# Optimization experiments

Measured on AMD Instinct MI355X. Metric: run time of the kernel, lower is better.

Reference implementation:

```python
import jax, jax.numpy as jnp
import numpy as np
import math

CHUNK = 128


def setup_inputs() -> dict:
    key = jax.random.key(0)
    ks = jax.random.split(key, 12)
    B, S, H, D = 2, 4096, 1024, 2048  # D = hidden_dim * expansion_factor
    std = 0.02
    inp = {
        "hidden_states": jax.random.normal(ks[0], (B, S, H), jnp.float32),
        "Wq": jax.random.normal(ks[1], (H, D), jnp.float32) * std,
        "bq": jnp.zeros((D,), jnp.float32),
        "Wk": jax.random.normal(ks[2], (H, D), jnp.float32) * std,
        "bk": jnp.zeros((D,), jnp.float32),
        "Wv": jax.random.normal(ks[3], (H, D), jnp.float32) * std,
        "bv": jnp.zeros((D,), jnp.float32),
        "Wg": jax.random.normal(ks[4], (H, D), jnp.float32) * std,
        "bg": jnp.zeros((D,), jnp.float32),
        "Wo": jax.random.normal(ks[5], (D, H), jnp.float32) * std,
        "bo": jnp.zeros((H,), jnp.float32),
    }
    return inp


def reference(hidden_states, Wq, bq, Wk, bk, Wv, bv, Wg, bg, Wo, bo):
    B, S, H = hidden_states.shape
    D = Wq.shape[1]
    cs = CHUNK
    nC = S // cs  # seq_len chosen as multiple of chunk_size (no padding path)

    q = hidden_states @ Wq + bq
    k = hidden_states @ Wk + bk
    v = hidden_states @ Wv + bv
    gate = jax.nn.sigmoid(hidden_states @ Wg + bg)

    qc = q.reshape(B, nC, cs, D)
    kc = k.reshape(B, nC, cs, D)
    vc = v.reshape(B, nC, cs, D)
    gc = gate.reshape(B, nC, cs, D)

    # intra-chunk causal softmax attention (vectorized over all chunks)
    scale = 1.0 / math.sqrt(D)
    attn = jnp.einsum('bncd,bnkd->bnck', qc, kc) * scale  # [B,nC,cs,cs]
    causal = jnp.tril(jnp.ones((cs, cs), bool))
    attn = jnp.where(causal, attn, -jnp.inf)
    attn = jax.nn.softmax(attn, axis=-1)
    local = jnp.einsum('bnck,bnkd->bncd', attn, vc)

    # inter-chunk linear-attention state accumulation:
    # cross_i = q_i @ sum_{j<i} K_j^T V_j  (sequential scan over chunks)
    def step(state, xs):
        qi, ki, vi = xs  # each [B,cs,D]
        cross = jnp.einsum('bcd,bde->bce', qi, state)
        state = state + jnp.einsum('bcd,bce->bde', ki, vi)
        return state, cross

    state0 = jnp.zeros((B, D, D), hidden_states.dtype)
    _, cross = jax.lax.scan(
        step, state0,
        (qc.transpose(1, 0, 2, 3), kc.transpose(1, 0, 2, 3), vc.transpose(1, 0, 2, 3)))
    cross = cross.transpose(1, 0, 2, 3)  # [B,nC,cs,D]

    out = (local + cross) * gc
    out = out.reshape(B, S, D)
    return out @ Wo + bo
```

## Files before the change

kernel.cpp:

```cpp
#include <hip/hip_runtime.h>
#include <hip/hip_bf16.h>
#include <math.h>


typedef __bf16 bf16_t;
typedef __bf16 bf16x8 __attribute__((ext_vector_type(8)));
typedef __bf16 bf16x4 __attribute__((ext_vector_type(4)));
typedef float f32x4 __attribute__((ext_vector_type(4)));

#define NB_ 2
#define SEQ 4096
#define HID 1024
#define DD 2048
#define BS 8192
#define LDS_CORE 98304
#define SP 264

__device__ __forceinline__ void async16(const void* g, void* l) {
  __builtin_amdgcn_global_load_lds(
      (const __attribute__((address_space(1))) void*)g,
      (__attribute__((address_space(3))) void*)l, 16, 0, 0);
}

#define VMW(n) asm volatile("s_waitcnt vmcnt(" #n ")" ::: "memory")
#define BARR __builtin_amdgcn_s_barrier()
#define FEN asm volatile("" ::: "memory")

template <int MFH>
__device__ __forceinline__ void readA8(const bf16_t* bufA, int aBase, int s0, int s1,
                                       bf16x8 (&af)[4][2]) {
#pragma unroll
  for (int mm = 0; mm < 4; ++mm) {
    int p = aBase + MFH * 8192 + mm * 1024;
    af[mm][0] = *reinterpret_cast<const bf16x8*>(&bufA[p + s0]);
    af[mm][1] = *reinterpret_cast<const bf16x8*>(&bufA[p + s1]);
  }
}
template <int NFH>
__device__ __forceinline__ void readB4(const bf16_t* bufB, int bBase, int s0, int s1,
                                       bf16x8 (&bv)[2][2]) {
#pragma unroll
  for (int nn = 0; nn < 2; ++nn) {
    int p = bBase + NFH * 8192 + nn * 1024;
    bv[nn][0] = *reinterpret_cast<const bf16x8*>(&bufB[p + s0]);
    bv[nn][1] = *reinterpret_cast<const bf16x8*>(&bufB[p + s1]);
  }
}
template <int MROWS, int MQ, int NQ>
__device__ __forceinline__ void mfmaQ(const bf16x8 (&af)[4][2], const bf16x8 (&bv)[2][2],
                                      f32x4 (&acc)[MROWS][4]) {
  __builtin_amdgcn_s_setprio(1);
#pragma unroll
  for (int kki = 0; kki < 2; ++kki)
#pragma unroll
    for (int mm = 0; mm < 4; ++mm)
#pragma unroll
      for (int nn = 0; nn < 2; ++nn)
        acc[MQ * 4 + mm][NQ * 2 + nn] = __builtin_amdgcn_mfma_f32_16x16x32_bf16(
            af[mm][kki], bv[nn][kki], acc[MQ * 4 + mm][NQ * 2 + nn], 0, 0, 0);
  __builtin_amdgcn_s_setprio(0);
}

__device__ __forceinline__ void core128(const bf16_t* __restrict__ A, int lda,
                                        const bf16_t* __restrict__ B, int ldb, int nt,
                                        bf16_t* lds, f32x4 (&acc)[4][4]) {
  const int t = threadIdx.x;
  const int lane = t & 63, w = t >> 6;
  const int wm = w >> 2, wn = w & 3;
  const int lr = lane & 15, lg = lane >> 4;
  const int xm = lr & 7;
  const int aBase = (wm * 64 + lr) * 64;
  const int bBase = (wn * 32 + lr) * 64;
  const int s0 = (lg ^ xm) * 8, s1 = ((4 + lg) ^ xm) * 8;
  const int slog = ((t & 7) ^ ((t >> 3) & 7)) * 8;
  int srcA[2], srcB[4];
#pragma unroll
  for (int blk = 0; blk < 2; ++blk) srcA[blk] = (blk * 64 + (t >> 3)) * lda + slog;
#pragma unroll
  for (int blk = 0; blk < 4; ++blk) {
    int prB = (blk << 6) + (t >> 3);
    int rB = (((prB >> 5) & 3) << 6) + ((prB >> 7) << 5) + (prB & 31);
    srcB[blk] = rB * ldb + slog;
  }
  const int dstT = t * 8;
#pragma unroll
  for (int m = 0; m < 4; ++m)
#pragma unroll
    for (int n = 0; n < 4; ++n) acc[m][n] = (f32x4){0.f, 0.f, 0.f, 0.f};

  {
    bf16_t* nA = lds;
    bf16_t* nB = lds + 8192;
    async16(A + srcA[0], nA + dstT);
    async16(A + srcA[1], nA + 4096 + dstT);
    async16(B + srcB[0], nB + dstT);
    async16(B + srcB[1], nB + 4096 + dstT);
    async16(B + srcB[2], nB + 8192 + dstT);
    async16(B + srcB[3], nB + 12288 + dstT);
  }
  bf16x8 af[4][2], bv0[2][2], bv1[2][2];
  for (int kt = 0; kt < nt; ++kt) {
    bf16_t* bufA = lds + (kt & 1) * 24576;
    bf16_t* bufB = bufA + 8192;
    bf16_t* nA = lds + ((kt + 1) & 1) * 24576;
    bf16_t* nB = nA + 8192;
    const int kn = (kt + 1 < nt ? kt + 1 : 0) << 6;
    const bf16_t* An = A + kn;
    const bf16_t* Bn = B + kn;
    VMW(2); BARR; FEN;
    readA8<0>(bufA, aBase, s0, s1, af);
    readB4<0>(bufB, bBase, s0, s1, bv0);
    async16(An + srcA[0], nA + dstT);
    async16(An + srcA[1], nA + 4096 + dstT);
    async16(Bn + srcB[0], nB + dstT);
    mfmaQ<4, 0, 0>(af, bv0, acc);
    VMW(3); BARR; FEN;
    readB4<1>(bufB, bBase, s0, s1, bv1);
    async16(Bn + srcB[1], nB + 4096 + dstT);
    async16(Bn + srcB[2], nB + 8192 + dstT);
    async16(Bn + srcB[3], nB + 12288 + dstT);
    mfmaQ<4, 0, 1>(af, bv1, acc);
  }
  VMW(0);
  BARR;
}

__global__ void k_cvt(const float4* __restrict__ in, bf16x4* __restrict__ out, int n4) {
  int i = blockIdx.x * blockDim.x + threadIdx.x;
  if (i < n4) {
    float4 v = in[i];
    bf16x4 o;
    o[0] = (bf16_t)v.x; o[1] = (bf16_t)v.y; o[2] = (bf16_t)v.z; o[3] = (bf16_t)v.w;
    out[i] = o;
  }
}

__global__ void k_tconv(const float* __restrict__ in, bf16_t* __restrict__ out,
                        int R, int C) {
  __shared__ bf16_t tile[64][65];
  int bc = blockIdx.x, br = blockIdx.y;
  int t = threadIdx.x;
  int c = t & 63, r0 = t >> 6;
#pragma unroll
  for (int rr = 0; rr < 64; rr += 4) {
    int r = rr + r0;
    tile[r][c] = (bf16_t)in[(long)(br * 64 + r) * C + bc * 64 + c];
  }
  __syncthreads();
#pragma unroll
  for (int rr = 0; rr < 64; rr += 4) {
    int r = rr + r0;
    out[(long)(bc * 64 + r) * R + br * 64 + c] = tile[c][r];
  }
}

__global__ void k_tbf16(const bf16_t* __restrict__ in, bf16_t* __restrict__ out,
                        int R, int C) {
  __shared__ bf16_t tile[64][65];
  long zoff = (long)blockIdx.z * R * C;
  in += zoff;
  out += zoff;
  int bc = blockIdx.x, br = blockIdx.y;
  int t = threadIdx.x;
  int c = t & 63, r0 = t >> 6;
#pragma unroll
  for (int rr = 0; rr < 64; rr += 4) {
    int r = rr + r0;
    tile[r][c] = in[(long)(br * 64 + r) * C + bc * 64 + c];
  }
  __syncthreads();
#pragma unroll
  for (int rr = 0; rr < 64; rr += 4) {
    int r = rr + r0;
    out[(long)(bc * 64 + r) * R + br * 64 + c] = tile[c][r];
  }
}

__global__ __launch_bounds__(512, 2) void k_gemm_qkvg(
    const bf16_t* __restrict__ hsb, const bf16_t* __restrict__ Wt4,
    const float* __restrict__ bq, const float* __restrict__ bk,
    const float* __restrict__ bv, const float* __restrict__ bg,
    bf16_t* __restrict__ out) {
  extern __shared__ bf16_t lds[];
  int c = blockIdx.x;
  int r = c >> 9, xj = c & 511;
  int xcd = xj & 7, j = xj >> 3;
  int mb = r * 16 + (xcd & 1) * 8 + (j & 7);
  int nb = (xcd >> 1) * 8 + (j >> 3);
  f32x4 acc[4][4];
  core128(hsb + (long)mb * 128 * HID, HID, Wt4 + (long)nb * 256 * HID, HID,
          HID / 64, lds, acc);
  const int t = threadIdx.x, lane = t & 63, w = t >> 6;
  const int wm = w >> 2, wn = w & 3, lr = lane & 15, lg = lane >> 4;
  int z = nb >> 3;
  const float* bias = z == 0 ? bq : z == 1 ? bk : z == 2 ? bv : bg;
  int colT = (nb & 7) * 256;
  float b4[4];
#pragma unroll
  for (int nf = 0; nf < 4; ++nf) b4[nf] = bias[colT + wn * 64 + nf * 16 + lr];
#pragma unroll
  for (int mf = 0; mf < 4; ++mf)
#pragma unroll
    for (int reg = 0; reg < 4; ++reg) {
      int lrow = wm * 64 + mf * 16 + lg * 4 + reg;
#pragma unroll
      for (int nf = 0; nf < 4; ++nf) {
        float v = acc[mf][nf][reg] + b4[nf];
        if (z == 3) v = 1.f / (1.f + __expf(-v));
        lds[lrow * SP + wn * 64 + nf * 16 + lr] = (bf16_t)v;
      }
    }
  __syncthreads();
  bf16_t* O = out + (long)z * BS * DD + (long)mb * 128 * DD + colT;
#pragma unroll
  for (int it = 0; it < 8; ++it) {
    int s = it * 512 + t;
    int rr2 = s >> 5, sg = s & 31;
    bf16x8 v = *reinterpret_cast<const bf16x8*>(&lds[rr2 * SP + sg * 8]);
    *reinterpret_cast<bf16x8*>(&O[(long)rr2 * DD + sg * 8]) = v;
  }
}

__global__ __launch_bounds__(512, 2) void k_pair(const bf16_t* __restrict__ Q,
                                                 const bf16_t* __restrict__ Kb,
                                                 bf16_t* __restrict__ P) {
  extern __shared__ bf16_t lds[];
  int p = blockIdx.x, b = blockIdx.y;
  int c = 0, base = 0;
  while (base + (c >> 1) + 1 <= p) { base += (c >> 1) + 1; ++c; }
  int jt = p - base;
  f32x4 acc[4][4];
  core128(Q + ((long)b * SEQ + (long)c * 128) * DD, DD,
          Kb + ((long)b * SEQ + (long)jt * 256) * DD, DD, DD / 64, lds, acc);
  const int t = threadIdx.x, lane = t & 63, w = t >> 6;
  const int wm = w >> 2, wn = w & 3, lr = lane & 15, lg = lane >> 4;
  bf16_t* Pt = P + ((long)b * SEQ + (long)c * 128) * (long)SEQ + (long)jt * 256;
  const bool hasDiag = (jt == (c >> 1));
  const int side = c & 1;
  const float scale = 0.02209708691207961f;
#pragma unroll
  for (int mf = 0; mf < 4; ++mf)
#pragma unroll
    for (int reg = 0; reg < 4; ++reg) {
      int lrow = wm * 64 + mf * 16 + lg * 4 + reg;
#pragma unroll
      for (int nf = 0; nf < 4; ++nf) {
        int col = wn * 64 + nf * 16 + lr;
        float v = acc[mf][nf][reg];
        if (hasDiag && (((col >> 7) == side) || side == 0)) v = 0.f;
        lds[lrow * SP + col] = (bf16_t)v;
      }
    }
  __syncthreads();
#pragma unroll
  for (int it = 0; it < 8; ++it) {
    int s = it * 512 + t;
    int rr2 = s >> 5, sg = s & 31;
    bf16x8 v = *reinterpret_cast<const bf16x8*>(&lds[rr2 * SP + sg * 8]);
    *reinterpret_cast<bf16x8*>(&Pt[(long)rr2 * SEQ + sg * 8]) = v;
  }
  if (hasDiag) {
    VMW(0);
    __syncthreads();
    float* smf = (float*)lds;
#pragma unroll
    for (int mf = 0; mf < 4; ++mf)
#pragma unroll
      for (int reg = 0; reg < 4; ++reg) {
        int row = wm * 64 + mf * 16 + lg * 4 + reg;
#pragma unroll
        for (int nf = 0; nf < 4; ++nf) {
          int col = wn * 64 + nf * 16 + lr;
          if ((col >> 7) == side) {
            int cc = col & 127;
            float sv = acc[mf][nf][reg] * scale;
            smf[row * 128 + ((cc + row) & 127)] = (cc <= row) ? sv : -1e30f;
          }
        }
      }
    __syncthreads();
    if (t < 128) {
      int r = t;
      float mx = -1e30f;
      for (int cc = 0; cc <= r; ++cc) mx = fmaxf(mx, smf[r * 128 + ((cc + r) & 127)]);
      float s = 0.f;
      for (int cc = 0; cc <= r; ++cc) s += __expf(smf[r * 128 + ((cc + r) & 127)] - mx);
      float inv = 1.f / s;
      for (int cc = 0; cc < 128; ++cc) {
        float v = (cc <= r) ? __expf(smf[r * 128 + ((cc + r) & 127)] - mx) * inv : 0.f;
        Pt[(long)r * SEQ + side * 128 + cc] = (bf16_t)v;
      }
    }
  }
}

__global__ __launch_bounds__(512, 2) void k_gemm2(const bf16_t* __restrict__ P,
                                                  const bf16_t* __restrict__ Vt,
                                                  const bf16_t* __restrict__ G,
                                                  bf16_t* __restrict__ OutPre) {
  extern __shared__ bf16_t lds[];
  int bid = blockIdx.x;
  int mq = 31 - (bid >> 4);
  int r2 = bid & 15;
  int nb = r2 >> 1, b = r2 & 1;
  f32x4 acc[4][4];
  core128(P + ((long)b * SEQ + (long)mq * 128) * (long)SEQ, SEQ,
          Vt + (long)b * DD * SEQ + (long)nb * 256 * SEQ, SEQ, (mq + 1) * 2, lds, acc);
  const int t = threadIdx.x, lane = t & 63, w = t >> 6;
  const int wm = w >> 2, wn = w & 3, lr = lane & 15, lg = lane >> 4;
  long rowb = (long)b * SEQ + (long)mq * 128;
#pragma unroll
  for (int mf = 0; mf < 4; ++mf)
#pragma unroll
    for (int reg = 0; reg < 4; ++reg) {
      int lrow = wm * 64 + mf * 16 + lg * 4 + reg;
#pragma unroll
      for (int nf = 0; nf < 4; ++nf) {
        int col = wn * 64 + nf * 16 + lr;
        float g = (float)G[(rowb + lrow) * DD + nb * 256 + col];
        lds[lrow * SP + col] = (bf16_t)(acc[mf][nf][reg] * g);
      }
    }
  __syncthreads();
  bf16_t* O = OutPre + rowb * DD + nb * 256;
#pragma unroll
  for (int it = 0; it < 8; ++it) {
    int s = it * 512 + t;
    int rr2 = s >> 5, sg = s & 31;
    bf16x8 v = *reinterpret_cast<const bf16x8*>(&lds[rr2 * SP + sg * 8]);
    *reinterpret_cast<bf16x8*>(&O[(long)rr2 * DD + sg * 8]) = v;
  }
}

__global__ __launch_bounds__(512, 2) void k_gemm3(const bf16_t* __restrict__ OutPre,
                                                  const bf16_t* __restrict__ Wot,
                                                  const float* __restrict__ bo,
                                                  float* __restrict__ out) {
  extern __shared__ bf16_t lds[];
  int mb = blockIdx.x >> 2, nb = blockIdx.x & 3;
  f32x4 acc[4][4];
  core128(OutPre + (long)mb * 128 * DD, DD, Wot + (long)nb * 256 * DD, DD,
          DD / 64, lds, acc);
  const int t = threadIdx.x, lane = t & 63, w = t >> 6;
  const int wm = w >> 2, wn = w & 3, lr = lane & 15, lg = lane >> 4;
  int colbase = nb * 256 + wn * 64;
  float b4[4];
#pragma unroll
  for (int nf = 0; nf < 4; ++nf) b4[nf] = bo[colbase + nf * 16 + lr];
#pragma unroll
  for (int mf = 0; mf < 4; ++mf)
#pragma unroll
    for (int reg = 0; reg < 4; ++reg) {
      long row = mb * 128 + wm * 64 + mf * 16 + lg * 4 + reg;
#pragma unroll
      for (int nf = 0; nf < 4; ++nf)
        out[row * HID + colbase + nf * 16 + lr] = acc[mf][nf][reg] + b4[nf];
    }
}

extern "C" void kernel_launch(void* const* d_in, const int* in_sizes, int n_in,
                              void* d_out, int out_size, void* d_ws, size_t ws_size,
                              hipStream_t stream) {
  const float* hs = (const float*)d_in[0];
  const float* Wq = (const float*)d_in[1];
  const float* bq = (const float*)d_in[2];
  const float* Wk = (const float*)d_in[3];
  const float* bk = (const float*)d_in[4];
  const float* Wv = (const float*)d_in[5];
  const float* bv = (const float*)d_in[6];
  const float* Wg = (const float*)d_in[7];
  const float* bg = (const float*)d_in[8];
  const float* Wo = (const float*)d_in[9];
  const float* bo = (const float*)d_in[10];
  float* out = (float*)d_out;

  char* ws = (char*)d_ws;
  const size_t MB = 1024 * 1024;
  bf16_t* P = (bf16_t*)(ws);
  bf16_t* hsb = (bf16_t*)(ws);
  bf16_t* Wt4 = (bf16_t*)(ws + 16 * MB);
  bf16_t* Wot = (bf16_t*)(ws + 64 * MB);
  bf16_t* QKVG = (bf16_t*)(ws + 68 * MB);
  bf16_t* Vt = (bf16_t*)(ws + 196 * MB);

  bf16_t* Qb = QKVG;
  bf16_t* Kbuf = QKVG + (long)BS * DD;
  bf16_t* Vbuf = QKVG + 2l * BS * DD;
  bf16_t* Gbuf = QKVG + 3l * BS * DD;
  bf16_t* OutPre = Vbuf;

  hipFuncSetAttribute((const void*)k_gemm_qkvg,
                      hipFuncAttributeMaxDynamicSharedMemorySize, LDS_CORE);
  hipFuncSetAttribute((const void*)k_pair,
                      hipFuncAttributeMaxDynamicSharedMemorySize, LDS_CORE);
  hipFuncSetAttribute((const void*)k_gemm2,
                      hipFuncAttributeMaxDynamicSharedMemorySize, LDS_CORE);
  hipFuncSetAttribute((const void*)k_gemm3,
                      hipFuncAttributeMaxDynamicSharedMemorySize, LDS_CORE);

  k_cvt<<<(BS * HID / 4 + 255) / 256, 256, 0, stream>>>((const float4*)hs,
                                                        (bf16x4*)hsb, BS * HID / 4);
  k_tconv<<<dim3(DD / 64, HID / 64), 256, 0, stream>>>(Wq, Wt4 + 0l * DD * HID, HID, DD);
  k_tconv<<<dim3(DD / 64, HID / 64), 256, 0, stream>>>(Wk, Wt4 + 1l * DD * HID, HID, DD);
  k_tconv<<<dim3(DD / 64, HID / 64), 256, 0, stream>>>(Wv, Wt4 + 2l * DD * HID, HID, DD);
  k_tconv<<<dim3(DD / 64, HID / 64), 256, 0, stream>>>(Wg, Wt4 + 3l * DD * HID, HID, DD);
  k_tconv<<<dim3(HID / 64, DD / 64), 256, 0, stream>>>(Wo, Wot, DD, HID);

  k_gemm_qkvg<<<2048, 512, LDS_CORE, stream>>>(hsb, Wt4, bq, bk, bv, bg, QKVG);

  k_tbf16<<<dim3(DD / 64, SEQ / 64, NB_), 256, 0, stream>>>(Vbuf, Vt, SEQ, DD);

  k_pair<<<dim3(272, 2), 512, LDS_CORE, stream>>>(Qb, Kbuf, P);

  k_gemm2<<<512, 512, LDS_CORE, stream>>>(P, Vt, Gbuf, OutPre);

  k_gemm3<<<256, 512, LDS_CORE, stream>>>(OutPre, Wot, bo, out);
}
```

Baseline: 446.6 us.

## Replace GEMM core with templated K=32 double-buffered core and retile all kernels

Replaces the 128x256 K=64 split-barrier GEMM core with a templated K=32 double-buffered core and retiles every kernel to match: QKVG uses 256x128 tiles, pair uses 128x128 tiles with 256 threads, and gemm2 uses 256x128 tiles. The V transpose moves into the QKVG epilogue, which removes a separate kernel. Diagonal softmax now runs in place in bf16 LDS. Smaller LDS footprints with launch bounds of 4 aim for higher occupancy, at the cost of shorter K steps, more barriers and a full vmcnt(0) wait every iteration.

```diff
diff --git a/kernel.cpp b/kernel.cpp
--- a/kernel.cpp
+++ b/kernel.cpp
@@ -13,8 +13,6 @@
 #define HID 1024
 #define DD 2048
 #define BS 8192
-#define LDS_CORE 98304
-#define SP 264
 
 __device__ __forceinline__ void async16(const void* g, void* l) {
   __builtin_amdgcn_global_load_lds(
@@ -22,107 +20,83 @@
       (__attribute__((address_space(3))) void*)l, 16, 0, 0);
 }
 
-#define VMW(n) asm volatile("s_waitcnt vmcnt(" #n ")" ::: "memory")
+#define VMW0 asm volatile("s_waitcnt vmcnt(0)" ::: "memory")
 #define BARR __builtin_amdgcn_s_barrier()
 #define FEN asm volatile("" ::: "memory")
 
-template <int MFH>
-__device__ __forceinline__ void readA8(const bf16_t* bufA, int aBase, int s0, int s1,
-                                       bf16x8 (&af)[4][2]) {
-#pragma unroll
-  for (int mm = 0; mm < 4; ++mm) {
-    int p = aBase + MFH * 8192 + mm * 1024;
-    af[mm][0] = *reinterpret_cast<const bf16x8*>(&bufA[p + s0]);
-    af[mm][1] = *reinterpret_cast<const bf16x8*>(&bufA[p + s1]);
-  }
-}
-template <int NFH>
-__device__ __forceinline__ void readB4(const bf16_t* bufB, int bBase, int s0, int s1,
-                                       bf16x8 (&bv)[2][2]) {
-#pragma unroll
-  for (int nn = 0; nn < 2; ++nn) {
-    int p = bBase + NFH * 8192 + nn * 1024;
-    bv[nn][0] = *reinterpret_cast<const bf16x8*>(&bufB[p + s0]);
-    bv[nn][1] = *reinterpret_cast<const bf16x8*>(&bufB[p + s1]);
-  }
-}
-template <int MROWS, int MQ, int NQ>
-__device__ __forceinline__ void mfmaQ(const bf16x8 (&af)[4][2], const bf16x8 (&bv)[2][2],
-                                      f32x4 (&acc)[MROWS][4]) {
-  __builtin_amdgcn_s_setprio(1);
-#pragma unroll
-  for (int kki = 0; kki < 2; ++kki)
-#pragma unroll
-    for (int mm = 0; mm < 4; ++mm)
-#pragma unroll
-      for (int nn = 0; nn < 2; ++nn)
-        acc[MQ * 4 + mm][NQ * 2 + nn] = __builtin_amdgcn_mfma_f32_16x16x32_bf16(
-            af[mm][kki], bv[nn][kki], acc[MQ * 4 + mm][NQ * 2 + nn], 0, 0, 0);
-  __builtin_amdgcn_s_setprio(0);
-}
-
-__device__ __forceinline__ void core128(const bf16_t* __restrict__ A, int lda,
+template <int WM, int WN>
+__device__ __forceinline__ void coreK32(const bf16_t* __restrict__ A, int lda,
                                         const bf16_t* __restrict__ B, int ldb, int nt,
                                         bf16_t* lds, f32x4 (&acc)[4][4]) {
+  constexpr int T = WM * WN * 64;
+  constexpr int AE = WM * 64 * 32;
+  constexpr int BE = WN * 64 * 32;
+  constexpr int BUF = AE + BE;
+  constexpr int NISS = BUF / (T * 8);
   const int t = threadIdx.x;
   const int lane = t & 63, w = t >> 6;
-  const int wm = w >> 2, wn = w & 3;
+  const int wm = w / WN, wn = w % WN;
   const int lr = lane & 15, lg = lane >> 4;
-  const int xm = lr & 7;
-  const int aBase = (wm * 64 + lr) * 64;
-  const int bBase = (wn * 32 + lr) * 64;
-  const int s0 = (lg ^ xm) * 8, s1 = ((4 + lg) ^ xm) * 8;
-  const int slog = ((t & 7) ^ ((t >> 3) & 7)) * 8;
-  int srcA[2], srcB[4];
-#pragma unroll
-  for (int blk = 0; blk < 2; ++blk) srcA[blk] = (blk * 64 + (t >> 3)) * lda + slog;
-#pragma unroll
-  for (int blk = 0; blk < 4; ++blk) {
-    int prB = (blk << 6) + (t >> 3);
-    int rB = (((prB >> 5) & 3) << 6) + ((prB >> 7) << 5) + (prB & 31);
-    srcB[blk] = rB * ldb + slog;
-  }
-  const int dstT = t * 8;
+
+  int aOff[4], bOff[4];
+#pragma unroll
+  for (int f = 0; f < 4; ++f) {
+    int ra = wm * 64 + f * 16 + lr;
+    aOff[f] = ra * 32 + (((lg + (ra >> 1)) & 3) << 3);
+    int rb = wn * 64 + f * 16 + lr;
+    bOff[f] = AE + rb * 32 + (((lg + (rb >> 1)) & 3) << 3);
+  }
+  int src[NISS];
+#pragma unroll
+  for (int q = 0; q < NISS; ++q) {
+    constexpr int ebase0 = 0;
+    int e = q * T * 8 + t * 8;
+    bool isB = (q * T * 8) >= AE;
+    int e2 = isB ? e - AE : e;
+    int r = e2 >> 5;
+    int g = (((e2 >> 3) & 3) - (r >> 1)) & 3;
+    src[q] = r * (isB ? ldb : lda) + g * 8;
+    (void)ebase0;
+  }
 #pragma unroll
   for (int m = 0; m < 4; ++m)
 #pragma unroll
     for (int n = 0; n < 4; ++n) acc[m][n] = (f32x4){0.f, 0.f, 0.f, 0.f};
 
   {
-    bf16_t* nA = lds;
-    bf16_t* nB = lds + 8192;
-    async16(A + srcA[0], nA + dstT);
-    async16(A + srcA[1], nA + 4096 + dstT);
-    async16(B + srcB[0], nB + dstT);
-    async16(B + srcB[1], nB + 4096 + dstT);
-    async16(B + srcB[2], nB + 8192 + dstT);
-    async16(B + srcB[3], nB + 12288 + dstT);
-  }
-  bf16x8 af[4][2], bv0[2][2], bv1[2][2];
-  for (int kt = 0; kt < nt; ++kt) {
-    bf16_t* bufA = lds + (kt & 1) * 24576;
-    bf16_t* bufB = bufA + 8192;
-    bf16_t* nA = lds + ((kt + 1) & 1) * 24576;
-    bf16_t* nB = nA + 8192;
-    const int kn = (kt + 1 < nt ? kt + 1 : 0) << 6;
-    const bf16_t* An = A + kn;
-    const bf16_t* Bn = B + kn;
-    VMW(2); BARR; FEN;
-    readA8<0>(bufA, aBase, s0, s1, af);
-    readB4<0>(bufB, bBase, s0, s1, bv0);
-    async16(An + srcA[0], nA + dstT);
-    async16(An + srcA[1], nA + 4096 + dstT);
-    async16(Bn + srcB[0], nB + dstT);
-    mfmaQ<4, 0, 0>(af, bv0, acc);
-    VMW(3); BARR; FEN;
-    readB4<1>(bufB, bBase, s0, s1, bv1);
-    async16(Bn + srcB[1], nB + 4096 + dstT);
-    async16(Bn + srcB[2], nB + 8192 + dstT);
-    async16(Bn + srcB[3], nB + 12288 + dstT);
-    mfmaQ<4, 0, 1>(af, bv1, acc);
-  }
-  VMW(0);
-  BARR;
+    bf16_t* buf0 = lds;
+#pragma unroll
+    for (int q = 0; q < NISS; ++q) {
+      bool isB = (q * T * 8) >= AE;
+      async16((isB ? B : A) + src[q], buf0 + q * T * 8 + t * 8);
+    }
+  }
+  VMW0; BARR; FEN;
+
+  for (int tt = 0; tt < nt; ++tt) {
+    bf16_t* cur = lds + (tt & 1) * BUF;
+    bf16_t* nxt = lds + ((tt + 1) & 1) * BUF;
+    const int kn = (tt + 1 < nt ? tt + 1 : 0) << 5;
+#pragma unroll
+    for (int q = 0; q < NISS; ++q) {
+      bool isB = (q * T * 8) >= AE;
+      async16((isB ? B : A) + kn + src[q], nxt + q * T * 8 + t * 8);
+    }
+    bf16x8 af[4], bv[4];
+#pragma unroll
+    for (int f = 0; f < 4; ++f) af[f] = *reinterpret_cast<const bf16x8*>(&cur[aOff[f]]);
+#pragma unroll
+    for (int f = 0; f < 4; ++f) bv[f] = *reinterpret_cast<const bf16x8*>(&cur[bOff[f]]);
+    __builtin_amdgcn_s_setprio(1);
+#pragma unroll
+    for (int mf = 0; mf < 4; ++mf)
+#pragma unroll
+      for (int nf = 0; nf < 4; ++nf)
+        acc[mf][nf] =
+            __builtin_amdgcn_mfma_f32_16x16x32_bf16(af[mf], bv[nf], acc[mf][nf], 0, 0, 0);
+    __builtin_amdgcn_s_setprio(0);
+    VMW0; BARR; FEN;
+  }
 }
 
 __global__ void k_cvt(const float4* __restrict__ in, bf16x4* __restrict__ out, int n4) {
@@ -154,47 +128,25 @@
   }
 }
 
-__global__ void k_tbf16(const bf16_t* __restrict__ in, bf16_t* __restrict__ out,
-                        int R, int C) {
-  __shared__ bf16_t tile[64][65];
-  long zoff = (long)blockIdx.z * R * C;
-  in += zoff;
-  out += zoff;
-  int bc = blockIdx.x, br = blockIdx.y;
-  int t = threadIdx.x;
-  int c = t & 63, r0 = t >> 6;
-#pragma unroll
-  for (int rr = 0; rr < 64; rr += 4) {
-    int r = rr + r0;
-    tile[r][c] = in[(long)(br * 64 + r) * C + bc * 64 + c];
-  }
-  __syncthreads();
-#pragma unroll
-  for (int rr = 0; rr < 64; rr += 4) {
-    int r = rr + r0;
-    out[(long)(bc * 64 + r) * R + br * 64 + c] = tile[c][r];
-  }
-}
-
-__global__ __launch_bounds__(512, 2) void k_gemm_qkvg(
+__global__ __launch_bounds__(512, 4) void k_gemm_qkvg(
     const bf16_t* __restrict__ hsb, const bf16_t* __restrict__ Wt4,
     const float* __restrict__ bq, const float* __restrict__ bk,
     const float* __restrict__ bv, const float* __restrict__ bg,
-    bf16_t* __restrict__ out) {
+    bf16_t* __restrict__ out, bf16_t* __restrict__ Vt) {
   extern __shared__ bf16_t lds[];
-  int c = blockIdx.x;
-  int r = c >> 9, xj = c & 511;
-  int xcd = xj & 7, j = xj >> 3;
-  int mb = r * 16 + (xcd & 1) * 8 + (j & 7);
-  int nb = (xcd >> 1) * 8 + (j >> 3);
+  const int SP = 136;
+  int i = blockIdx.x;
+  int xcd = i & 7, g = i >> 3;
+  int mb = g >> 3;
+  int nb = xcd * 8 + (g & 7);
   f32x4 acc[4][4];
-  core128(hsb + (long)mb * 128 * HID, HID, Wt4 + (long)nb * 256 * HID, HID,
-          HID / 64, lds, acc);
+  coreK32<4, 2>(hsb + (long)mb * 256 * HID, HID, Wt4 + (long)nb * 128 * HID, HID,
+                HID / 32, lds, acc);
   const int t = threadIdx.x, lane = t & 63, w = t >> 6;
-  const int wm = w >> 2, wn = w & 3, lr = lane & 15, lg = lane >> 4;
-  int z = nb >> 3;
+  const int wm = w >> 1, wn = w & 1, lr = lane & 15, lg = lane >> 4;
+  int z = nb >> 4;
   const float* bias = z == 0 ? bq : z == 1 ? bk : z == 2 ? bv : bg;
-  int colT = (nb & 7) * 256;
+  int colT = (nb & 15) * 128;
   float b4[4];
 #pragma unroll
   for (int nf = 0; nf < 4; ++nf) b4[nf] = bias[colT + wn * 64 + nf * 16 + lr];
@@ -211,104 +163,112 @@
       }
     }
   __syncthreads();
-  bf16_t* O = out + (long)z * BS * DD + (long)mb * 128 * DD + colT;
-#pragma unroll
-  for (int it = 0; it < 8; ++it) {
-    int s = it * 512 + t;
-    int rr2 = s >> 5, sg = s & 31;
-    bf16x8 v = *reinterpret_cast<const bf16x8*>(&lds[rr2 * SP + sg * 8]);
-    *reinterpret_cast<bf16x8*>(&O[(long)rr2 * DD + sg * 8]) = v;
-  }
-}
-
-__global__ __launch_bounds__(512, 2) void k_pair(const bf16_t* __restrict__ Q,
+  if (z != 2) {
+    bf16_t* O = out + (long)z * BS * DD + (long)mb * 256 * DD + colT;
+#pragma unroll
+    for (int it = 0; it < 8; ++it) {
+      int s = it * 512 + t;
+      int row = s >> 4, sg = s & 15;
+      bf16x8 v = *reinterpret_cast<const bf16x8*>(&lds[row * SP + sg * 8]);
+      *reinterpret_cast<bf16x8*>(&O[(long)row * DD + sg * 8]) = v;
+    }
+  } else {
+    int bz = mb >> 4, smb = mb & 15;
+    bf16_t* Vd = Vt + ((long)bz * DD + colT) * SEQ + smb * 256;
+#pragma unroll
+    for (int it = 0; it < 8; ++it) {
+      int d = (t >> 3) + (it & 1) * 64;
+      int s8 = (t & 7) * 8 + (it >> 1) * 64;
+      bf16x8 v;
+#pragma unroll
+      for (int j = 0; j < 8; ++j) v[j] = lds[(s8 + j) * SP + d];
+      *reinterpret_cast<bf16x8*>(&Vd[(long)d * SEQ + s8]) = v;
+    }
+  }
+}
+
+__global__ __launch_bounds__(256, 4) void k_pair(const bf16_t* __restrict__ Q,
                                                  const bf16_t* __restrict__ Kb,
                                                  bf16_t* __restrict__ P) {
   extern __shared__ bf16_t lds[];
+  const int SP = 136;
   int p = blockIdx.x, b = blockIdx.y;
   int c = 0, base = 0;
-  while (base + (c >> 1) + 1 <= p) { base += (c >> 1) + 1; ++c; }
+  while (base + c + 1 <= p) { base += c + 1; ++c; }
   int jt = p - base;
   f32x4 acc[4][4];
-  core128(Q + ((long)b * SEQ + (long)c * 128) * DD, DD,
-          Kb + ((long)b * SEQ + (long)jt * 256) * DD, DD, DD / 64, lds, acc);
+  coreK32<2, 2>(Q + ((long)b * SEQ + (long)c * 128) * DD, DD,
+                Kb + ((long)b * SEQ + (long)jt * 128) * DD, DD, DD / 32, lds, acc);
   const int t = threadIdx.x, lane = t & 63, w = t >> 6;
-  const int wm = w >> 2, wn = w & 3, lr = lane & 15, lg = lane >> 4;
-  bf16_t* Pt = P + ((long)b * SEQ + (long)c * 128) * (long)SEQ + (long)jt * 256;
-  const bool hasDiag = (jt == (c >> 1));
-  const int side = c & 1;
+  const int wm = w >> 1, wn = w & 1, lr = lane & 15, lg = lane >> 4;
+  bf16_t* Pt = P + ((long)b * SEQ + (long)c * 128) * (long)SEQ + (long)jt * 128;
+  const bool diag = (jt == c);
   const float scale = 0.02209708691207961f;
 #pragma unroll
   for (int mf = 0; mf < 4; ++mf)
 #pragma unroll
     for (int reg = 0; reg < 4; ++reg) {
-      int lrow = wm * 64 + mf * 16 + lg * 4 + reg;
+      int row = wm * 64 + mf * 16 + lg * 4 + reg;
 #pragma unroll
       for (int nf = 0; nf < 4; ++nf) {
         int col = wn * 64 + nf * 16 + lr;
         float v = acc[mf][nf][reg];
-        if (hasDiag && (((col >> 7) == side) || side == 0)) v = 0.f;
-        lds[lrow * SP + col] = (bf16_t)v;
+        if (diag) v = (col <= row) ? v * scale : -1e30f;
+        lds[row * SP + col] = (bf16_t)v;
       }
     }
   __syncthreads();
-#pragma unroll
-  for (int it = 0; it < 8; ++it) {
-    int s = it * 512 + t;
-    int rr2 = s >> 5, sg = s & 31;
-    bf16x8 v = *reinterpret_cast<const bf16x8*>(&lds[rr2 * SP + sg * 8]);
-    *reinterpret_cast<bf16x8*>(&Pt[(long)rr2 * SEQ + sg * 8]) = v;
-  }
-  if (hasDiag) {
-    VMW(0);
-    __syncthreads();
-    float* smf = (float*)lds;
-#pragma unroll
-    for (int mf = 0; mf < 4; ++mf)
-#pragma unroll
-      for (int reg = 0; reg < 4; ++reg) {
-        int row = wm * 64 + mf * 16 + lg * 4 + reg;
-#pragma unroll
-        for (int nf = 0; nf < 4; ++nf) {
-          int col = wn * 64 + nf * 16 + lr;
-          if ((col >> 7) == side) {
-            int cc = col & 127;
-            float sv = acc[mf][nf][reg] * scale;
-            smf[row * 128 + ((cc + row) & 127)] = (cc <= row) ? sv : -1e30f;
-          }
-        }
-      }
-    __syncthreads();
+  if (diag) {
     if (t < 128) {
       int r = t;
+      bf16_t* rowp = lds + r * SP;
       float mx = -1e30f;
-      for (int cc = 0; cc <= r; ++cc) mx = fmaxf(mx, smf[r * 128 + ((cc + r) & 127)]);
-      float s = 0.f;
-      for (int cc = 0; cc <= r; ++cc) s += __expf(smf[r * 128 + ((cc + r) & 127)] - mx);
-      float inv = 1.f / s;
+      for (int cc = 0; cc <= r; ++cc) mx = fmaxf(mx, (float)rowp[cc]);
+      float ssum = 0.f;
+      for (int cc = 0; cc <= r; ++cc) ssum += __expf((float)rowp[cc] - mx);
+      float inv = 1.f / ssum;
       for (int cc = 0; cc < 128; ++cc) {
-        float v = (cc <= r) ? __expf(smf[r * 128 + ((cc + r) & 127)] - mx) * inv : 0.f;
-        Pt[(long)r * SEQ + side * 128 + cc] = (bf16_t)v;
+        float v = (cc <= r) ? __expf((float)rowp[cc] - mx) * inv : 0.f;
+        rowp[cc] = (bf16_t)v;
       }
     }
-  }
-}
-
-__global__ __launch_bounds__(512, 2) void k_gemm2(const bf16_t* __restrict__ P,
+    __syncthreads();
+  }
+#pragma unroll
+  for (int it = 0; it < 8; ++it) {
+    int s = it * 256 + t;
+    int row = s >> 4, sg = s & 15;
+    bf16x8 v = *reinterpret_cast<const bf16x8*>(&lds[row * SP + sg * 8]);
+    *reinterpret_cast<bf16x8*>(&Pt[(long)row * SEQ + sg * 8]) = v;
+  }
+  if (diag && !(c & 1)) {
+    bf16x8 zv = {};
+#pragma unroll
+    for (int it = 0; it < 8; ++it) {
+      int s = it * 256 + t;
+      int row = s >> 4, sg = s & 15;
+      *reinterpret_cast<bf16x8*>(&Pt[(long)row * SEQ + 128 + sg * 8]) = zv;
+    }
+  }
+}
+
+__global__ __launch_bounds__(512, 4) void k_gemm2(const bf16_t* __restrict__ P,
                                                   const bf16_t* __restrict__ Vt,
                                                   const bf16_t* __restrict__ G,
                                                   bf16_t* __restrict__ OutPre) {
   extern __shared__ bf16_t lds[];
+  const int SP = 136;
   int bid = blockIdx.x;
-  int mq = 31 - (bid >> 4);
-  int r2 = bid & 15;
-  int nb = r2 >> 1, b = r2 & 1;
+  int ip = 15 - (bid >> 5);
+  int r2 = bid & 31;
+  int nb = r2 >> 1, b2 = r2 & 1;
   f32x4 acc[4][4];
-  core128(P + ((long)b * SEQ + (long)mq * 128) * (long)SEQ, SEQ,
-          Vt + (long)b * DD * SEQ + (long)nb * 256 * SEQ, SEQ, (mq + 1) * 2, lds, acc);
+  coreK32<4, 2>(P + ((long)b2 * SEQ + (long)ip * 256) * (long)SEQ, SEQ,
+                Vt + (long)b2 * DD * SEQ + (long)nb * 128 * SEQ, SEQ, (ip + 1) * 8,
+                lds, acc);
   const int t = threadIdx.x, lane = t & 63, w = t >> 6;
-  const int wm = w >> 2, wn = w & 3, lr = lane & 15, lg = lane >> 4;
-  long rowb = (long)b * SEQ + (long)mq * 128;
+  const int wm = w >> 1, wn = w & 1, lr = lane & 15, lg = lane >> 4;
+  long rowb = (long)b2 * SEQ + (long)ip * 256;
 #pragma unroll
   for (int mf = 0; mf < 4; ++mf)
 #pragma unroll
@@ -317,30 +277,30 @@
 #pragma unroll
       for (int nf = 0; nf < 4; ++nf) {
         int col = wn * 64 + nf * 16 + lr;
-        float g = (float)G[(rowb + lrow) * DD + nb * 256 + col];
-        lds[lrow * SP + col] = (bf16_t)(acc[mf][nf][reg] * g);
+        float gg = (float)G[(rowb + lrow) * DD + nb * 128 + col];
+        lds[lrow * SP + col] = (bf16_t)(acc[mf][nf][reg] * gg);
       }
     }
   __syncthreads();
-  bf16_t* O = OutPre + rowb * DD + nb * 256;
+  bf16_t* O = OutPre + rowb * DD + nb * 128;
 #pragma unroll
   for (int it = 0; it < 8; ++it) {
     int s = it * 512 + t;
-    int rr2 = s >> 5, sg = s & 31;
-    bf16x8 v = *reinterpret_cast<const bf16x8*>(&lds[rr2 * SP + sg * 8]);
-    *reinterpret_cast<bf16x8*>(&O[(long)rr2 * DD + sg * 8]) = v;
-  }
-}
-
-__global__ __launch_bounds__(512, 2) void k_gemm3(const bf16_t* __restrict__ OutPre,
+    int row = s >> 4, sg = s & 15;
+    bf16x8 v = *reinterpret_cast<const bf16x8*>(&lds[row * SP + sg * 8]);
+    *reinterpret_cast<bf16x8*>(&O[(long)row * DD + sg * 8]) = v;
+  }
+}
+
+__global__ __launch_bounds__(512, 4) void k_gemm3(const bf16_t* __restrict__ OutPre,
                                                   const bf16_t* __restrict__ Wot,
                                                   const float* __restrict__ bo,
                                                   float* __restrict__ out) {
   extern __shared__ bf16_t lds[];
   int mb = blockIdx.x >> 2, nb = blockIdx.x & 3;
   f32x4 acc[4][4];
-  core128(OutPre + (long)mb * 128 * DD, DD, Wot + (long)nb * 256 * DD, DD,
-          DD / 64, lds, acc);
+  coreK32<2, 4>(OutPre + (long)mb * 128 * DD, DD, Wot + (long)nb * 256 * DD, DD,
+                DD / 32, lds, acc);
   const int t = threadIdx.x, lane = t & 63, w = t >> 6;
   const int wm = w >> 2, wn = w & 3, lr = lane & 15, lg = lane >> 4;
   int colbase = nb * 256 + wn * 64;
@@ -389,14 +349,18 @@
   bf16_t* Gbuf = QKVG + 3l * BS * DD;
   bf16_t* OutPre = Vbuf;
 
+  const int LDS_QKVG = 69632;
+  const int LDS_PAIR = 34816;
+  const int LDS_G2 = 69632;
+  const int LDS_G3 = 49152;
   hipFuncSetAttribute((const void*)k_gemm_qkvg,
-                      hipFuncAttributeMaxDynamicSharedMemorySize, LDS_CORE);
+                      hipFuncAttributeMaxDynamicSharedMemorySize, LDS_QKVG);
   hipFuncSetAttribute((const void*)k_pair,
-                      hipFuncAttributeMaxDynamicSharedMemorySize, LDS_CORE);
+                      hipFuncAttributeMaxDynamicSharedMemorySize, LDS_PAIR);
   hipFuncSetAttribute((const void*)k_gemm2,
-                      hipFuncAttributeMaxDynamicSharedMemorySize, LDS_CORE);
+                      hipFuncAttributeMaxDynamicSharedMemorySize, LDS_G2);
   hipFuncSetAttribute((const void*)k_gemm3,
-                      hipFuncAttributeMaxDynamicSharedMemorySize, LDS_CORE);
+                      hipFuncAttributeMaxDynamicSharedMemorySize, LDS_G3);
 
   k_cvt<<<(BS * HID / 4 + 255) / 256, 256, 0, stream>>>((const float4*)hs,
                                                         (bf16x4*)hsb, BS * HID / 4);
@@ -406,13 +370,11 @@
   k_tconv<<<dim3(DD / 64, HID / 64), 256, 0, stream>>>(Wg, Wt4 + 3l * DD * HID, HID, DD);
   k_tconv<<<dim3(HID / 64, DD / 64), 256, 0, stream>>>(Wo, Wot, DD, HID);
 
-  k_gemm_qkvg<<<2048, 512, LDS_CORE, stream>>>(hsb, Wt4, bq, bk, bv, bg, QKVG);
-
-  k_tbf16<<<dim3(DD / 64, SEQ / 64, NB_), 256, 0, stream>>>(Vbuf, Vt, SEQ, DD);
-
-  k_pair<<<dim3(272, 2), 512, LDS_CORE, stream>>>(Qb, Kbuf, P);
-
-  k_gemm2<<<512, 512, LDS_CORE, stream>>>(P, Vt, Gbuf, OutPre);
-
-  k_gemm3<<<256, 512, LDS_CORE, stream>>>(OutPre, Wot, bo, out);
-}
+  k_gemm_qkvg<<<2048, 512, LDS_QKVG, stream>>>(hsb, Wt4, bq, bk, bv, bg, QKVG, Vt);
+
+  k_pair<<<dim3(528, 2), 256, LDS_PAIR, stream>>>(Qb, Kbuf, P);
+
+  k_gemm2<<<512, 512, LDS_G2, stream>>>(P, Vt, Gbuf, OutPre);
+
+  k_gemm3<<<256, 512, LDS_G3, stream>>>(OutPre, Wot, bo, out);
+}
```

New measurement: 454.8 us. About the same (+1.8%).
